# Kernel optimization log

Hardware: AMD Instinct MI355X
Metric: run time of the kernel (lower is better)

## Reference

```python
import jax, jax.numpy as jnp
import numpy as np

D = 768
H = 12
DK = D // H
FF = 3072
EPS = 1e-5


def layernorm(x, g, b):
    mu = jnp.mean(x, axis=-1, keepdims=True)
    var = jnp.mean((x - mu) ** 2, axis=-1, keepdims=True)
    return (x - mu) * jax.lax.rsqrt(var + EPS) * g + b


def setup_inputs() -> dict:
    key = jax.random.key(0)
    ks = jax.random.split(key, 12)
    B, S = 4, 2048
    s = 0.02
    return {
        "embedding": jax.random.normal(ks[0], (B, S, D), jnp.float32),
        "mask": jnp.ones((B, 1, 1, S), jnp.int32),
        "Wq": jax.random.normal(ks[1], (D, D), jnp.float32) * s,
        "bq": jnp.zeros((D,), jnp.float32),
        "Wk": jax.random.normal(ks[2], (D, D), jnp.float32) * s,
        "bk": jnp.zeros((D,), jnp.float32),
        "Wv": jax.random.normal(ks[3], (D, D), jnp.float32) * s,
        "bv": jnp.zeros((D,), jnp.float32),
        "Wo": jax.random.normal(ks[4], (D, D), jnp.float32) * s,
        "bo": jnp.zeros((D,), jnp.float32),
        "W1": jax.random.normal(ks[5], (D, FF), jnp.float32) * s,
        "b1": jnp.zeros((FF,), jnp.float32),
        "W2": jax.random.normal(ks[6], (FF, D), jnp.float32) * s,
        "b2": jnp.zeros((D,), jnp.float32),
        "ln_g": jnp.ones((D,), jnp.float32),
        "ln_b": jnp.zeros((D,), jnp.float32),
    }


def reference(embedding, mask, Wq, bq, Wk, bk, Wv, bv, Wo, bo, W1, b1, W2, b2, ln_g, ln_b):
    B, S, _ = embedding.shape
    # QKV projections -> [B, H, S, DK]
    def split_heads(t):
        return t.reshape(B, S, H, DK).transpose(0, 2, 1, 3)
    q = split_heads(embedding @ Wq + bq)
    k = split_heads(embedding @ Wk + bk)
    v = split_heads(embedding @ Wv + bv)
    scores = jnp.einsum("bhqd,bhkd->bhqk", q, k) / jnp.sqrt(jnp.float32(DK))
    scores = jnp.where(mask == 0, jnp.float32(-1e9), scores)
    weights = jax.nn.softmax(scores, axis=-1)  # dropout = identity (eval)
    context = jnp.einsum("bhqk,bhkd->bhqd", weights, v)
    context = context.transpose(0, 2, 1, 3).reshape(B, S, D)
    attn_out = context @ Wo + bo
    x = layernorm(attn_out + embedding, ln_g, ln_b)
    ff = jax.nn.relu(x @ W1 + b1) @ W2 + b2
    return layernorm(x + ff, ln_g, ln_b)
```

## Files before the change

### kernel.cpp

```cpp
#include <hip/hip_runtime.h>

#define D_MODEL 768
#define NHEADS  12
#define SEQ     2048
#define BATCH   4
#define FF_DIM  3072
#define NTOK    (BATCH * SEQ)

typedef short short8 __attribute__((ext_vector_type(8)));
typedef float f32x4 __attribute__((ext_vector_type(4)));
typedef float f32x16 __attribute__((ext_vector_type(16)));
typedef int int4v __attribute__((ext_vector_type(4)));
typedef int int2v __attribute__((ext_vector_type(2)));
typedef unsigned short ushort4v __attribute__((ext_vector_type(4)));
typedef float float4v __attribute__((ext_vector_type(4)));

__device__ __forceinline__ short f2bf(float x) {
  unsigned u = __builtin_bit_cast(unsigned, x);
  u += 0x7fffu + ((u >> 16) & 1u);
  return (short)(u >> 16);
}
__device__ __forceinline__ float bf2f(short x) {
  return __builtin_bit_cast(float, ((unsigned)(unsigned short)x) << 16);
}
__device__ __forceinline__ int cvtpk(float a, float b) {
  int r;
  asm("v_cvt_pk_bf16_f32 %0, %1, %2" : "=v"(r) : "v"(a), "v"(b));
  return r;
}
__device__ __forceinline__ void gll16(const void* g, void* l) {
  __builtin_amdgcn_global_load_lds(
      (const __attribute__((address_space(1))) void*)g,
      (__attribute__((address_space(3))) void*)l, 16, 0, 0);
}

__device__ __forceinline__ void wt_tile(float (*T)[65], const float* __restrict__ W,
                                        short* __restrict__ Wt, int K, int N,
                                        int bx, int by, int t) {
  const int c = t & 63, rb = t >> 6;
  const int k0 = by * 64, n0 = bx * 64;
#pragma unroll
  for (int i = 0; i < 16; ++i) {
    const int r = rb * 16 + i;
    T[c][r] = W[(size_t)(k0 + r) * N + n0 + c];
  }
  __syncthreads();
#pragma unroll
  for (int j = 0; j < 16; ++j) {
    const int idx = t + j * 256;
    const int nl = idx >> 6, kl = idx & 63;
    Wt[(size_t)(n0 + nl) * K + k0 + kl] = f2bf(T[nl][kl]);
  }
}

__global__ __launch_bounds__(256) void prep(
    const float* __restrict__ Wq, const float* __restrict__ Wk, const float* __restrict__ Wv,
    const float* __restrict__ Wo, const float* __restrict__ W1, const float* __restrict__ W2,
    const float* __restrict__ bq, const float* __restrict__ bk, const float* __restrict__ bv,
    const float* __restrict__ emb,
    short* __restrict__ wqkvt, short* __restrict__ wot, short* __restrict__ w1t,
    short* __restrict__ w2t, float* __restrict__ bqkv, short* __restrict__ x0) {
  __shared__ float T[64][65];
  const int bi = blockIdx.x;
  const int t = threadIdx.x;
  if (bi < 432) {
    const int s = bi / 144, l = bi % 144;
    const float* W = (s == 0) ? Wq : (s == 1) ? Wk : Wv;
    wt_tile(T, W, wqkvt + (size_t)s * 768 * 768, 768, 768, l % 12, l / 12, t);
  } else if (bi < 576) {
    const int l = bi - 432;
    wt_tile(T, Wo, wot, 768, 768, l % 12, l / 12, t);
  } else if (bi < 1152) {
    const int l = bi - 576;
    wt_tile(T, W1, w1t, 768, 3072, l % 48, l / 48, t);
  } else if (bi < 1728) {
    const int l = bi - 1152;
    wt_tile(T, W2, w2t, 3072, 768, l % 12, l / 12, t);
  } else if (bi == 1728) {
#pragma unroll
    for (int j = 0; j < 9; ++j) {
      const int i = t + j * 256;
      bqkv[i] = (i < 768) ? bq[i] : (i < 1536) ? bk[i - 768] : bv[i - 1536];
    }
  } else {
    const int i = (bi - 1729) * 256 + t;
    float4v v = *(const float4v*)(emb + (size_t)i * 4);
    ushort4v p;
    p[0] = (unsigned short)f2bf(v[0]);
    p[1] = (unsigned short)f2bf(v[1]);
    p[2] = (unsigned short)f2bf(v[2]);
    p[3] = (unsigned short)f2bf(v[3]);
    *(ushort4v*)(x0 + (size_t)i * 4) = p;
  }
}

enum { EPI_QKV = 0, EPI_WO = 1, EPI_RELU = 2, EPI_FF = 3 };

template <int EPI>
__global__ __launch_bounds__(256) void gemm_bt(const short* __restrict__ A,
                                               const short* __restrict__ Bt,
                                               const float* __restrict__ bias,
                                               const float* __restrict__ extraF,
                                               const short* __restrict__ extraB,
                                               void* __restrict__ outp,
                                               int M, int N, int K) {
  __shared__ short As[128 * 64];
  __shared__ short Bs[128 * 64];
  const int tid = threadIdx.x;
  const int lane = tid & 63, wid = tid >> 6;
  const int wr = wid >> 1, wc = wid & 1;
  const int l16 = lane & 15, lg = lane >> 4;
  const int brow = blockIdx.y * 128, bcol = blockIdx.x * 128;

  f32x4 acc[4][4];
#pragma unroll
  for (int i = 0; i < 4; ++i)
#pragma unroll
    for (int j = 0; j < 4; ++j) acc[i][j] = (f32x4){0.f, 0.f, 0.f, 0.f};

  for (int kt = 0; kt < K; kt += 64) {
    __syncthreads();
#pragma unroll
    for (int i = 0; i < 4; ++i) {
      const int c = wid * 256 + i * 64 + lane;
      const int row = c >> 3;
      const int gc = (c & 7) ^ (row & 7);
      gll16(A + (size_t)(brow + row) * K + kt + gc * 8,
            (char*)As + (wid * 256 + i * 64) * 16);
      gll16(Bt + (size_t)(bcol + row) * K + kt + gc * 8,
            (char*)Bs + (wid * 256 + i * 64) * 16);
    }
    __syncthreads();
#pragma unroll
    for (int kc = 0; kc < 2; ++kc) {
      short8 af[4], bfr[4];
#pragma unroll
      for (int m = 0; m < 4; ++m) {
        const int row = wr * 64 + m * 16 + l16;
        const int ch = (kc * 4 + lg) ^ (row & 7);
        af[m] = *(const short8*)((const char*)As + row * 128 + ch * 16);
      }
#pragma unroll
      for (int n = 0; n < 4; ++n) {
        const int row = wc * 64 + n * 16 + l16;
        const int ch = (kc * 4 + lg) ^ (row & 7);
        bfr[n] = *(const short8*)((const char*)Bs + row * 128 + ch * 16);
      }
#pragma unroll
      for (int m = 0; m < 4; ++m)
#pragma unroll
        for (int n = 0; n < 4; ++n)
          acc[m][n] = __builtin_amdgcn_mfma_f32_16x16x32_bf16(af[m], bfr[n],
                                                              acc[m][n], 0, 0, 0);
    }
  }

  const int mbase = brow + wr * 64;
  const int nbase = bcol + wc * 64;

  if constexpr (EPI == EPI_QKV) {
    short* qb_ = (short*)outp;
    short* kb_ = qb_ + (size_t)NTOK * D_MODEL;
    short* vt_ = kb_ + (size_t)NTOK * D_MODEL;
    const int type = nbase / 768;
#pragma unroll
    for (int ni = 0; ni < 4; ++ni) {
      const int n = nbase + ni * 16 + l16;
      const float bv = bias[n];
      const int ncol = n - type * 768;
      const int h = ncol >> 6, dk = ncol & 63;
      if (type == 2) {
#pragma unroll
        for (int mi = 0; mi < 4; ++mi) {
          const int m0 = mbase + mi * 16 + lg * 4;
          const int bidx = m0 >> 11, s0 = m0 & 2047;
          ushort4v pk;
#pragma unroll
          for (int r = 0; r < 4; ++r) pk[r] = (unsigned short)f2bf(acc[mi][ni][r] + bv);
          *(ushort4v*)(vt_ + (((size_t)bidx * NHEADS + h) * 64 + dk) * SEQ + s0) = pk;
        }
      } else {
        short* o = (type == 0) ? qb_ : kb_;
        const float sc = (type == 0) ? 0.125f * 1.44269504f : 1.f;
#pragma unroll
        for (int mi = 0; mi < 4; ++mi) {
#pragma unroll
          for (int r = 0; r < 4; ++r) {
            const int m = mbase + mi * 16 + lg * 4 + r;
            const int bidx = m >> 11, sidx = m & 2047;
            o[(((size_t)bidx * NHEADS + h) * SEQ + sidx) * 64 + dk] =
                f2bf((acc[mi][ni][r] + bv) * sc);
          }
        }
      }
    }
  } else if constexpr (EPI == EPI_WO) {
    short* o = (short*)outp;
#pragma unroll
    for (int ni = 0; ni < 4; ++ni) {
      const int n = nbase + ni * 16 + l16;
      const float bv = bias[n];
#pragma unroll
      for (int mi = 0; mi < 4; ++mi)
#pragma unroll
        for (int r = 0; r < 4; ++r) {
          const int m = mbase + mi * 16 + lg * 4 + r;
          const size_t idx = (size_t)m * N + n;
          o[idx] = f2bf(acc[mi][ni][r] + bv + extraF[idx]);
        }
    }
  } else if constexpr (EPI == EPI_FF) {
    short* o = (short*)outp;
#pragma unroll
    for (int ni = 0; ni < 4; ++ni) {
      const int n = nbase + ni * 16 + l16;
      const float bv = bias[n];
#pragma unroll
      for (int mi = 0; mi < 4; ++mi)
#pragma unroll
        for (int r = 0; r < 4; ++r) {
          const int m = mbase + mi * 16 + lg * 4 + r;
          const size_t idx = (size_t)m * N + n;
          o[idx] = f2bf(acc[mi][ni][r] + bv + bf2f(extraB[idx]));
        }
    }
  } else {
    short* o = (short*)outp;
#pragma unroll
    for (int ni = 0; ni < 4; ++ni) {
      const int n = nbase + ni * 16 + l16;
      const float bv = bias[n];
#pragma unroll
      for (int mi = 0; mi < 4; ++mi)
#pragma unroll
        for (int r = 0; r < 4; ++r) {
          const int m = mbase + mi * 16 + lg * 4 + r;
          o[(size_t)m * N + n] = f2bf(fmaxf(acc[mi][ni][r] + bv, 0.f));
        }
    }
  }
}

__global__ __launch_bounds__(256, 3) void attn_fa2(
    const short* __restrict__ Q,
    const short* __restrict__ Kb,
    const short* __restrict__ Vt,
    const int* __restrict__ mask,
    short* __restrict__ ctx) {
  __shared__ short KsA[64 * 64], KsB[64 * 64];
  __shared__ short VsA[64 * 64], VsB[64 * 64];
  __shared__ float bc[4][32];
  const int tid = threadIdx.x;
  const int lane = tid & 63, w = tid >> 6;
  const int l31 = lane & 31, hi = lane >> 5;
  const int bh = blockIdx.y, b = bh / NHEADS, h = bh % NHEADS;
  const int q0 = blockIdx.x * 128 + w * 32;

  const short* qp = Q + ((size_t)bh * SEQ + q0 + l31) * 64;
  short8 qf[4];
#pragma unroll
  for (int s = 0; s < 4; ++s) qf[s] = *(const short8*)(qp + s * 16 + hi * 8);

  short8 vones;
#pragma unroll
  for (int i = 0; i < 8; ++i) vones[i] = (short)0x3F80;

  f32x16 o0, o1, o2;
#pragma unroll
  for (int i = 0; i < 16; ++i) { o0[i] = 0.f; o1[i] = 0.f; o2[i] = 0.f; }
  float m = -1e30f;

  auto stage = [&](short* Ksd, short* Vsd, int kv0) {
#pragma unroll
    for (int i = 0; i < 2; ++i) {
      const int c = i * 256 + tid;
      const int row = c >> 3, ch = c & 7;
      const int gc = ch ^ (row & 7);
      gll16(Kb + ((size_t)bh * SEQ + kv0 + row) * 64 + gc * 8,
            (char*)Ksd + (i * 256 + w * 64) * 16);
      gll16(Vt + ((size_t)bh * 64 + row) * SEQ + kv0 + gc * 8,
            (char*)Vsd + (i * 256 + w * 64) * 16);
    }
  };

  stage(KsA, VsA, 0);
  __syncthreads();

  for (int t = 0; t < SEQ / 64; ++t) {
    const short* Ksc = (t & 1) ? KsB : KsA;
    const short* Vsc = (t & 1) ? VsB : VsA;

    f32x16 s0, s1;
#pragma unroll
    for (int i = 0; i < 16; ++i) { s0[i] = 0.f; s1[i] = 0.f; }
#pragma unroll
    for (int slot = 0; slot < 4; ++slot) {
      const int ch0 = (slot * 2 + hi) ^ (l31 & 7);
      short8 a0 = *(const short8*)((const char*)Ksc + l31 * 128 + ch0 * 16);
      s0 = __builtin_amdgcn_mfma_f32_32x32x16_bf16(a0, qf[slot], s0, 0, 0, 0);
      short8 a1 = *(const short8*)((const char*)Ksc + (32 + l31) * 128 + ch0 * 16);
      s1 = __builtin_amdgcn_mfma_f32_32x32x16_bf16(a1, qf[slot], s1, 0, 0, 0);
    }

    if (t + 1 < SEQ / 64)
      stage((t & 1) ? KsA : KsB, (t & 1) ? VsA : VsB, (t + 1) * 64);

    const int mv = mask[(size_t)b * SEQ + t * 64 + lane];
    if (__any(mv == 0)) {
#pragma unroll
      for (int r = 0; r < 16; ++r) {
        const int cr = (r & 3) + 8 * (r >> 2) + 4 * hi;
        if (__shfl(mv, cr) == 0) s0[r] = -1e9f;
        if (__shfl(mv, 32 + cr) == 0) s1[r] = -1e9f;
      }
    }

    float pmax = fmaxf(s0[0], s0[1]);
#pragma unroll
    for (int r = 2; r < 16; r += 2) pmax = fmaxf(pmax, fmaxf(s0[r], s0[r + 1]));
#pragma unroll
    for (int r = 0; r < 16; r += 2) pmax = fmaxf(pmax, fmaxf(s1[r], s1[r + 1]));
    pmax = fmaxf(pmax, __shfl_xor(pmax, 32));
    if (!__all(pmax - m <= 11.0f)) {
      const float mn = fmaxf(m, pmax);
      const float corr = exp2f(m - mn);
      if (lane < 32) bc[w][l31] = corr;
#pragma unroll
      for (int r = 0; r < 16; ++r) {
        const float cf = bc[w][(r & 3) + 8 * (r >> 2) + 4 * hi];
        o0[r] *= cf;
        o1[r] *= cf;
        o2[r] *= cf;
      }
      m = mn;
    }
#pragma unroll
    for (int r = 0; r < 16; ++r) {
      s0[r] = exp2f(s0[r] - m);
      s1[r] = exp2f(s1[r] - m);
    }

#pragma unroll
    for (int c = 0; c < 2; ++c) {
      const f32x16 sc = c ? s1 : s0;
#pragma unroll
      for (int ks = 0; ks < 2; ++ks) {
        const int rb = ks * 8;
        int x0_ = cvtpk(sc[rb + 0], sc[rb + 1]);
        int y0_ = cvtpk(sc[rb + 4], sc[rb + 5]);
        int x1_ = cvtpk(sc[rb + 2], sc[rb + 3]);
        int y1_ = cvtpk(sc[rb + 6], sc[rb + 7]);
        int4v pw;
#if __has_builtin(__builtin_amdgcn_permlane32_swap)
        int2v r0 = __builtin_amdgcn_permlane32_swap(x0_, y0_, false, false);
        int2v r1 = __builtin_amdgcn_permlane32_swap(x1_, y1_, false, false);
        pw[0] = r0[0]; pw[1] = r1[0]; pw[2] = r0[1]; pw[3] = r1[1];
#else
        const int ys0 = __shfl_xor(y0_, 32);
        const int xs0 = __shfl_xor(x0_, 32);
        const int ys1 = __shfl_xor(y1_, 32);
        const int xs1 = __shfl_xor(x1_, 32);
        pw[0] = hi ? ys0 : x0_;
        pw[1] = hi ? ys1 : x1_;
        pw[2] = hi ? y0_ : xs0;
        pw[3] = hi ? y1_ : xs1;
#endif
        const short8 pa = __builtin_bit_cast(short8, pw);
        const int vslot = c * 2 + ks;
        {
          const int vch = (vslot * 2 + hi) ^ (l31 & 7);
          short8 vb0 = *(const short8*)((const char*)Vsc + l31 * 128 + vch * 16);
          o0 = __builtin_amdgcn_mfma_f32_32x32x16_bf16(pa, vb0, o0, 0, 0, 0);
          short8 vb1 = *(const short8*)((const char*)Vsc + (32 + l31) * 128 + vch * 16);
          o1 = __builtin_amdgcn_mfma_f32_32x32x16_bf16(pa, vb1, o1, 0, 0, 0);
        }
        o2 = __builtin_amdgcn_mfma_f32_32x32x16_bf16(pa, vones, o2, 0, 0, 0);
      }
    }
    __syncthreads();
  }

#pragma unroll
  for (int r = 0; r < 16; ++r) {
    const int q = (r & 3) + 8 * (r >> 2) + 4 * hi;
    const float inv = 1.f / o2[r];
    short* cp = ctx + ((size_t)b * SEQ + q0 + q) * D_MODEL + h * 64;
    cp[l31] = f2bf(o0[r] * inv);
    cp[32 + l31] = f2bf(o1[r] * inv);
  }
}

template <int OUT_F32>
__global__ __launch_bounds__(256) void ln_w(const short* __restrict__ y,
                                            const float* __restrict__ gw,
                                            const float* __restrict__ bw,
                                            float* __restrict__ of,
                                            short* __restrict__ ob) {
  const int lane = threadIdx.x & 63, w = threadIdx.x >> 6;
  const int row = blockIdx.x * 4 + w;
  const short* yr = y + (size_t)row * D_MODEL;
  short8 v8 = *(const short8*)(yr + lane * 8);
  ushort4v v4 = *(const ushort4v*)(yr + 512 + lane * 4);
  float f[12];
#pragma unroll
  for (int j = 0; j < 8; ++j) f[j] = bf2f(v8[j]);
#pragma unroll
  for (int j = 0; j < 4; ++j) f[8 + j] = bf2f((short)v4[j]);
  float s = 0.f, q = 0.f;
#pragma unroll
  for (int j = 0; j < 12; ++j) { s += f[j]; q += f[j] * f[j]; }
#pragma unroll
  for (int mm = 1; mm < 64; mm <<= 1) {
    s += __shfl_xor(s, mm);
    q += __shfl_xor(q, mm);
  }
  const float mu = s * (1.f / D_MODEL);
  const float rs = rsqrtf(q * (1.f / D_MODEL) - mu * mu + 1e-5f);
  float4v g0 = *(const float4v*)(gw + lane * 8);
  float4v g1 = *(const float4v*)(gw + lane * 8 + 4);
  float4v g2 = *(const float4v*)(gw + 512 + lane * 4);
  float4v b0 = *(const float4v*)(bw + lane * 8);
  float4v b1 = *(const float4v*)(bw + lane * 8 + 4);
  float4v b2 = *(const float4v*)(bw + 512 + lane * 4);
  float o[12];
#pragma unroll
  for (int j = 0; j < 4; ++j) o[j] = (f[j] - mu) * rs * g0[j] + b0[j];
#pragma unroll
  for (int j = 0; j < 4; ++j) o[4 + j] = (f[4 + j] - mu) * rs * g1[j] + b1[j];
#pragma unroll
  for (int j = 0; j < 4; ++j) o[8 + j] = (f[8 + j] - mu) * rs * g2[j] + b2[j];
  if constexpr (OUT_F32) {
    float* orow = of + (size_t)row * D_MODEL;
    float4v t0, t1, t2;
#pragma unroll
    for (int j = 0; j < 4; ++j) { t0[j] = o[j]; t1[j] = o[4 + j]; t2[j] = o[8 + j]; }
    *(float4v*)(orow + lane * 8) = t0;
    *(float4v*)(orow + lane * 8 + 4) = t1;
    *(float4v*)(orow + 512 + lane * 4) = t2;
  } else {
    short* orow = ob + (size_t)row * D_MODEL;
    ushort4v t0, t1, t2;
#pragma unroll
    for (int j = 0; j < 4; ++j) {
      t0[j] = (unsigned short)f2bf(o[j]);
      t1[j] = (unsigned short)f2bf(o[4 + j]);
      t2[j] = (unsigned short)f2bf(o[8 + j]);
    }
    *(ushort4v*)(orow + lane * 8) = t0;
    *(ushort4v*)(orow + lane * 8 + 4) = t1;
    *(ushort4v*)(orow + 512 + lane * 4) = t2;
  }
}

extern "C" void kernel_launch(void* const* d_in, const int* in_sizes, int n_in,
                              void* d_out, int out_size, void* d_ws, size_t ws_size,
                              hipStream_t stream) {
  const float* emb = (const float*)d_in[0];
  const int* mask = (const int*)d_in[1];
  const float* Wq = (const float*)d_in[2];
  const float* bq = (const float*)d_in[3];
  const float* Wk = (const float*)d_in[4];
  const float* bk = (const float*)d_in[5];
  const float* Wv = (const float*)d_in[6];
  const float* bv = (const float*)d_in[7];
  const float* Wo = (const float*)d_in[8];
  const float* bo = (const float*)d_in[9];
  const float* W1 = (const float*)d_in[10];
  const float* b1 = (const float*)d_in[11];
  const float* W2 = (const float*)d_in[12];
  const float* b2 = (const float*)d_in[13];
  const float* lng = (const float*)d_in[14];
  const float* lnb = (const float*)d_in[15];

  char* ws = (char*)d_ws;
  size_t off = 0;
  auto alloc = [&](size_t bytes) -> char* {
    char* p = ws + off;
    off = (off + bytes + 255) & ~(size_t)255;
    return p;
  };
  const size_t DD = (size_t)D_MODEL * D_MODEL;
  const size_t DF = (size_t)D_MODEL * FF_DIM;
  const size_t TD = (size_t)NTOK * D_MODEL;
  const size_t TF = (size_t)NTOK * FF_DIM;

  short* wqkvt = (short*)alloc(3 * DD * 2);
  short* wot = (short*)alloc(DD * 2);
  short* w1t = (short*)alloc(DF * 2);
  short* w2t = (short*)alloc(DF * 2);
  float* bqkv = (float*)alloc(2304 * 4);
  short* x0 = (short*)alloc(TD * 2);
  short* qkv = (short*)alloc(3 * TD * 2);
  short* aresb = (short*)alloc(TD * 2);
  short* xbf = (short*)alloc(TD * 2);
  short* hbf = (short*)alloc(TF * 2);
  short* ffresb = (short*)alloc(TD * 2);
  short* qb = qkv;
  short* kb = qkv + TD;
  short* vtb = qkv + 2 * TD;
  short* ctx = x0;

  prep<<<dim3(1729 + (int)(TD / 1024)), 256, 0, stream>>>(
      Wq, Wk, Wv, Wo, W1, W2, bq, bk, bv, emb, wqkvt, wot, w1t, w2t, bqkv, x0);
  gemm_bt<EPI_QKV><<<dim3(18, 64), 256, 0, stream>>>(
      x0, wqkvt, bqkv, nullptr, nullptr, qkv, NTOK, 3 * D_MODEL, D_MODEL);
  attn_fa2<<<dim3(16, BATCH * NHEADS), 256, 0, stream>>>(qb, kb, vtb, mask, ctx);
  gemm_bt<EPI_WO><<<dim3(6, 64), 256, 0, stream>>>(
      ctx, wot, bo, emb, nullptr, aresb, NTOK, D_MODEL, D_MODEL);
  ln_w<0><<<dim3(NTOK / 4), 256, 0, stream>>>(aresb, lng, lnb, nullptr, xbf);
  gemm_bt<EPI_RELU><<<dim3(24, 64), 256, 0, stream>>>(
      xbf, w1t, b1, nullptr, nullptr, hbf, NTOK, FF_DIM, D_MODEL);
  gemm_bt<EPI_FF><<<dim3(6, 64), 256, 0, stream>>>(
      hbf, w2t, b2, nullptr, xbf, ffresb, NTOK, D_MODEL, FF_DIM);
  ln_w<1><<<dim3(NTOK / 4), 256, 0, stream>>>(ffresb, lng, lnb, (float*)d_out, nullptr);
}
```

Before: 306.5 us.

## Process 64 query rows per wave in attention to reuse K/V fragments

The attention kernel now uses 2 waves per block, each handling two 32-row query groups instead of one. Each K and V fragment read from shared memory feeds two MFMAs, which halves LDS traffic per FLOP and raises MFMA density per wave. The cost is roughly double the accumulator registers and fewer waves per CU (launch bounds 128,2), which reduces latency hiding. Each wave also issues more global-to-LDS staging loads.

```diff
diff --git a/kernel.cpp b/kernel.cpp
--- a/kernel.cpp
+++ b/kernel.cpp
@@ -241,7 +241,7 @@
   }
 }
 
-__global__ __launch_bounds__(256, 3) void attn_fa2(
+__global__ __launch_bounds__(128, 2) void attn_fa3(
     const short* __restrict__ Q,
     const short* __restrict__ Kb,
     const short* __restrict__ Vt,
@@ -249,37 +249,44 @@
     short* __restrict__ ctx) {
   __shared__ short KsA[64 * 64], KsB[64 * 64];
   __shared__ short VsA[64 * 64], VsB[64 * 64];
-  __shared__ float bc[4][32];
+  __shared__ float bc[2][2][32];
   const int tid = threadIdx.x;
   const int lane = tid & 63, w = tid >> 6;
   const int l31 = lane & 31, hi = lane >> 5;
   const int bh = blockIdx.y, b = bh / NHEADS, h = bh % NHEADS;
-  const int q0 = blockIdx.x * 128 + w * 32;
-
-  const short* qp = Q + ((size_t)bh * SEQ + q0 + l31) * 64;
-  short8 qf[4];
-#pragma unroll
-  for (int s = 0; s < 4; ++s) qf[s] = *(const short8*)(qp + s * 16 + hi * 8);
+  const int q0 = blockIdx.x * 128 + w * 64;
+
+  const short* qpA = Q + ((size_t)bh * SEQ + q0 + l31) * 64;
+  const short* qpB = qpA + 32 * 64;
+  short8 qfA[4], qfB[4];
+#pragma unroll
+  for (int s = 0; s < 4; ++s) {
+    qfA[s] = *(const short8*)(qpA + s * 16 + hi * 8);
+    qfB[s] = *(const short8*)(qpB + s * 16 + hi * 8);
+  }
 
   short8 vones;
 #pragma unroll
   for (int i = 0; i < 8; ++i) vones[i] = (short)0x3F80;
 
-  f32x16 o0, o1, o2;
-#pragma unroll
-  for (int i = 0; i < 16; ++i) { o0[i] = 0.f; o1[i] = 0.f; o2[i] = 0.f; }
-  float m = -1e30f;
+  f32x16 o0a, o1a, o2a, o0b, o1b, o2b;
+#pragma unroll
+  for (int i = 0; i < 16; ++i) {
+    o0a[i] = 0.f; o1a[i] = 0.f; o2a[i] = 0.f;
+    o0b[i] = 0.f; o1b[i] = 0.f; o2b[i] = 0.f;
+  }
+  float mA = -1e30f, mB = -1e30f;
 
   auto stage = [&](short* Ksd, short* Vsd, int kv0) {
 #pragma unroll
-    for (int i = 0; i < 2; ++i) {
-      const int c = i * 256 + tid;
-      const int row = c >> 3, ch = c & 7;
-      const int gc = ch ^ (row & 7);
+    for (int i = 0; i < 4; ++i) {
+      const int c = (i * 2 + w) * 64 + lane;
+      const int row = c >> 3;
+      const int gc = (c & 7) ^ (row & 7);
       gll16(Kb + ((size_t)bh * SEQ + kv0 + row) * 64 + gc * 8,
-            (char*)Ksd + (i * 256 + w * 64) * 16);
+            (char*)Ksd + ((i * 2 + w) * 64) * 16);
       gll16(Vt + ((size_t)bh * 64 + row) * SEQ + kv0 + gc * 8,
-            (char*)Vsd + (i * 256 + w * 64) * 16);
+            (char*)Vsd + ((i * 2 + w) * 64) * 16);
     }
   };
 
@@ -290,16 +297,18 @@
     const short* Ksc = (t & 1) ? KsB : KsA;
     const short* Vsc = (t & 1) ? VsB : VsA;
 
-    f32x16 s0, s1;
-#pragma unroll
-    for (int i = 0; i < 16; ++i) { s0[i] = 0.f; s1[i] = 0.f; }
+    f32x16 s0a, s1a, s0b, s1b;
+#pragma unroll
+    for (int i = 0; i < 16; ++i) { s0a[i] = 0.f; s1a[i] = 0.f; s0b[i] = 0.f; s1b[i] = 0.f; }
 #pragma unroll
     for (int slot = 0; slot < 4; ++slot) {
       const int ch0 = (slot * 2 + hi) ^ (l31 & 7);
       short8 a0 = *(const short8*)((const char*)Ksc + l31 * 128 + ch0 * 16);
-      s0 = __builtin_amdgcn_mfma_f32_32x32x16_bf16(a0, qf[slot], s0, 0, 0, 0);
       short8 a1 = *(const short8*)((const char*)Ksc + (32 + l31) * 128 + ch0 * 16);
-      s1 = __builtin_amdgcn_mfma_f32_32x32x16_bf16(a1, qf[slot], s1, 0, 0, 0);
+      s0a = __builtin_amdgcn_mfma_f32_32x32x16_bf16(a0, qfA[slot], s0a, 0, 0, 0);
+      s0b = __builtin_amdgcn_mfma_f32_32x32x16_bf16(a0, qfB[slot], s0b, 0, 0, 0);
+      s1a = __builtin_amdgcn_mfma_f32_32x32x16_bf16(a1, qfA[slot], s1a, 0, 0, 0);
+      s1b = __builtin_amdgcn_mfma_f32_32x32x16_bf16(a1, qfB[slot], s1b, 0, 0, 0);
     }
 
     if (t + 1 < SEQ / 64)
@@ -310,72 +319,86 @@
 #pragma unroll
       for (int r = 0; r < 16; ++r) {
         const int cr = (r & 3) + 8 * (r >> 2) + 4 * hi;
-        if (__shfl(mv, cr) == 0) s0[r] = -1e9f;
-        if (__shfl(mv, 32 + cr) == 0) s1[r] = -1e9f;
-      }
-    }
-
-    float pmax = fmaxf(s0[0], s0[1]);
-#pragma unroll
-    for (int r = 2; r < 16; r += 2) pmax = fmaxf(pmax, fmaxf(s0[r], s0[r + 1]));
-#pragma unroll
-    for (int r = 0; r < 16; r += 2) pmax = fmaxf(pmax, fmaxf(s1[r], s1[r + 1]));
-    pmax = fmaxf(pmax, __shfl_xor(pmax, 32));
-    if (!__all(pmax - m <= 11.0f)) {
-      const float mn = fmaxf(m, pmax);
-      const float corr = exp2f(m - mn);
-      if (lane < 32) bc[w][l31] = corr;
+        if (__shfl(mv, cr) == 0) { s0a[r] = -1e9f; s0b[r] = -1e9f; }
+        if (__shfl(mv, 32 + cr) == 0) { s1a[r] = -1e9f; s1b[r] = -1e9f; }
+      }
+    }
+
+    auto smax = [&](f32x16& s0, f32x16& s1, f32x16& o0, f32x16& o1, f32x16& o2,
+                    float& m, int g) {
+      float pmax = fmaxf(s0[0], s0[1]);
+#pragma unroll
+      for (int r = 2; r < 16; r += 2) pmax = fmaxf(pmax, fmaxf(s0[r], s0[r + 1]));
+#pragma unroll
+      for (int r = 0; r < 16; r += 2) pmax = fmaxf(pmax, fmaxf(s1[r], s1[r + 1]));
+      pmax = fmaxf(pmax, __shfl_xor(pmax, 32));
+      if (!__all(pmax - m <= 11.0f)) {
+        const float mn = fmaxf(m, pmax);
+        const float corr = exp2f(m - mn);
+        if (lane < 32) bc[w][g][l31] = corr;
+#pragma unroll
+        for (int r = 0; r < 16; ++r) {
+          const float cf = bc[w][g][(r & 3) + 8 * (r >> 2) + 4 * hi];
+          o0[r] *= cf;
+          o1[r] *= cf;
+          o2[r] *= cf;
+        }
+        m = mn;
+      }
 #pragma unroll
       for (int r = 0; r < 16; ++r) {
-        const float cf = bc[w][(r & 3) + 8 * (r >> 2) + 4 * hi];
-        o0[r] *= cf;
-        o1[r] *= cf;
-        o2[r] *= cf;
-      }
-      m = mn;
-    }
-#pragma unroll
-    for (int r = 0; r < 16; ++r) {
-      s0[r] = exp2f(s0[r] - m);
-      s1[r] = exp2f(s1[r] - m);
-    }
-
-#pragma unroll
-    for (int c = 0; c < 2; ++c) {
-      const f32x16 sc = c ? s1 : s0;
-#pragma unroll
-      for (int ks = 0; ks < 2; ++ks) {
-        const int rb = ks * 8;
-        int x0_ = cvtpk(sc[rb + 0], sc[rb + 1]);
-        int y0_ = cvtpk(sc[rb + 4], sc[rb + 5]);
-        int x1_ = cvtpk(sc[rb + 2], sc[rb + 3]);
-        int y1_ = cvtpk(sc[rb + 6], sc[rb + 7]);
-        int4v pw;
+        s0[r] = exp2f(s0[r] - m);
+        s1[r] = exp2f(s1[r] - m);
+      }
+    };
+    smax(s0a, s1a, o0a, o1a, o2a, mA, 0);
+    smax(s0b, s1b, o0b, o1b, o2b, mB, 1);
+
+    short8 paA[4], paB[4];
+#pragma unroll
+    for (int g = 0; g < 2; ++g) {
+#pragma unroll
+      for (int c = 0; c < 2; ++c) {
+        const f32x16 sc = g ? (c ? s1b : s0b) : (c ? s1a : s0a);
+#pragma unroll
+        for (int ks = 0; ks < 2; ++ks) {
+          const int rb = ks * 8;
+          int x0_ = cvtpk(sc[rb + 0], sc[rb + 1]);
+          int y0_ = cvtpk(sc[rb + 4], sc[rb + 5]);
+          int x1_ = cvtpk(sc[rb + 2], sc[rb + 3]);
+          int y1_ = cvtpk(sc[rb + 6], sc[rb + 7]);
+          int4v pw;
 #if __has_builtin(__builtin_amdgcn_permlane32_swap)
-        int2v r0 = __builtin_amdgcn_permlane32_swap(x0_, y0_, false, false);
-        int2v r1 = __builtin_amdgcn_permlane32_swap(x1_, y1_, false, false);
-        pw[0] = r0[0]; pw[1] = r1[0]; pw[2] = r0[1]; pw[3] = r1[1];
+          int2v r0 = __builtin_amdgcn_permlane32_swap(x0_, y0_, false, false);
+          int2v r1 = __builtin_amdgcn_permlane32_swap(x1_, y1_, false, false);
+          pw[0] = r0[0]; pw[1] = r1[0]; pw[2] = r0[1]; pw[3] = r1[1];
 #else
-        const int ys0 = __shfl_xor(y0_, 32);
-        const int xs0 = __shfl_xor(x0_, 32);
-        const int ys1 = __shfl_xor(y1_, 32);
-        const int xs1 = __shfl_xor(x1_, 32);
-        pw[0] = hi ? ys0 : x0_;
-        pw[1] = hi ? ys1 : x1_;
-        pw[2] = hi ? y0_ : xs0;
-        pw[3] = hi ? y1_ : xs1;
+          const int ys0 = __shfl_xor(y0_, 32);
+          const int xs0 = __shfl_xor(x0_, 32);
+          const int ys1 = __shfl_xor(y1_, 32);
+          const int xs1 = __shfl_xor(x1_, 32);
+          pw[0] = hi ? ys0 : x0_;
+          pw[1] = hi ? ys1 : x1_;
+          pw[2] = hi ? y0_ : xs0;
+          pw[3] = hi ? y1_ : xs1;
 #endif
-        const short8 pa = __builtin_bit_cast(short8, pw);
-        const int vslot = c * 2 + ks;
-        {
-          const int vch = (vslot * 2 + hi) ^ (l31 & 7);
-          short8 vb0 = *(const short8*)((const char*)Vsc + l31 * 128 + vch * 16);
-          o0 = __builtin_amdgcn_mfma_f32_32x32x16_bf16(pa, vb0, o0, 0, 0, 0);
-          short8 vb1 = *(const short8*)((const char*)Vsc + (32 + l31) * 128 + vch * 16);
-          o1 = __builtin_amdgcn_mfma_f32_32x32x16_bf16(pa, vb1, o1, 0, 0, 0);
-        }
-        o2 = __builtin_amdgcn_mfma_f32_32x32x16_bf16(pa, vones, o2, 0, 0, 0);
-      }
+          const short8 pa = __builtin_bit_cast(short8, pw);
+          if (g) paB[c * 2 + ks] = pa; else paA[c * 2 + ks] = pa;
+        }
+      }
+    }
+
+#pragma unroll
+    for (int vs = 0; vs < 4; ++vs) {
+      const int vch = (vs * 2 + hi) ^ (l31 & 7);
+      short8 vb0 = *(const short8*)((const char*)Vsc + l31 * 128 + vch * 16);
+      short8 vb1 = *(const short8*)((const char*)Vsc + (32 + l31) * 128 + vch * 16);
+      o0a = __builtin_amdgcn_mfma_f32_32x32x16_bf16(paA[vs], vb0, o0a, 0, 0, 0);
+      o0b = __builtin_amdgcn_mfma_f32_32x32x16_bf16(paB[vs], vb0, o0b, 0, 0, 0);
+      o1a = __builtin_amdgcn_mfma_f32_32x32x16_bf16(paA[vs], vb1, o1a, 0, 0, 0);
+      o1b = __builtin_amdgcn_mfma_f32_32x32x16_bf16(paB[vs], vb1, o1b, 0, 0, 0);
+      o2a = __builtin_amdgcn_mfma_f32_32x32x16_bf16(paA[vs], vones, o2a, 0, 0, 0);
+      o2b = __builtin_amdgcn_mfma_f32_32x32x16_bf16(paB[vs], vones, o2b, 0, 0, 0);
     }
     __syncthreads();
   }
@@ -383,10 +406,18 @@
 #pragma unroll
   for (int r = 0; r < 16; ++r) {
     const int q = (r & 3) + 8 * (r >> 2) + 4 * hi;
-    const float inv = 1.f / o2[r];
-    short* cp = ctx + ((size_t)b * SEQ + q0 + q) * D_MODEL + h * 64;
-    cp[l31] = f2bf(o0[r] * inv);
-    cp[32 + l31] = f2bf(o1[r] * inv);
+    {
+      const float inv = 1.f / o2a[r];
+      short* cp = ctx + ((size_t)b * SEQ + q0 + q) * D_MODEL + h * 64;
+      cp[l31] = f2bf(o0a[r] * inv);
+      cp[32 + l31] = f2bf(o1a[r] * inv);
+    }
+    {
+      const float inv = 1.f / o2b[r];
+      short* cp = ctx + ((size_t)b * SEQ + q0 + 32 + q) * D_MODEL + h * 64;
+      cp[l31] = f2bf(o0b[r] * inv);
+      cp[32 + l31] = f2bf(o1b[r] * inv);
+    }
   }
 }
 
@@ -504,7 +535,7 @@
       Wq, Wk, Wv, Wo, W1, W2, bq, bk, bv, emb, wqkvt, wot, w1t, w2t, bqkv, x0);
   gemm_bt<EPI_QKV><<<dim3(18, 64), 256, 0, stream>>>(
       x0, wqkvt, bqkv, nullptr, nullptr, qkv, NTOK, 3 * D_MODEL, D_MODEL);
-  attn_fa2<<<dim3(16, BATCH * NHEADS), 256, 0, stream>>>(qb, kb, vtb, mask, ctx);
+  attn_fa3<<<dim3(16, BATCH * NHEADS), 128, 0, stream>>>(qb, kb, vtb, mask, ctx);
   gemm_bt<EPI_WO><<<dim3(6, 64), 256, 0, stream>>>(
       ctx, wot, bo, emb, nullptr, aresb, NTOK, D_MODEL, D_MODEL);
   ln_w<0><<<dim3(NTOK / 4), 256, 0, stream>>>(aresb, lng, lnb, nullptr, xbf);
```

Measured after the change: 393.3 us. 1.28x slower.
